# Optimization experiments

Measured on AMD Instinct MI355X. Metric: run time of the kernel, lower is better.

The kernel has to match this reference:

```python
import jax, jax.numpy as jnp
import numpy as np

HDIM = 4
P = 2 ** HDIM  # 16 hypercube nodes


def build_dense_weight(hweight, out_features, in_features):
    # hweight: [hdim+1, P, ob, ib]; assemble dense [out_features, in_features]
    ob = out_features // P
    ib = in_features // P
    i = jnp.arange(P)
    w = jnp.zeros((P, P, ob, ib), dtype=hweight.dtype)
    # diagonal blocks: w[i, i] = hweight[0, i]
    w = w.at[i, i].set(hweight[0])
    # hypercube neighbor blocks: w[i ^ (1<<d), i] = hweight[d+1, i]
    for d in range(HDIM):
        j = i ^ (1 << d)
        w = w.at[j, i].set(hweight[d + 1])
    # permute (0,2,1,3) then reshape -> [out_features, in_features]
    w = jnp.transpose(w, (0, 2, 1, 3)).reshape(out_features, in_features)
    return w


def setup_inputs() -> dict:
    key = jax.random.key(0)
    k1, k2, k3 = jax.random.split(key, 3)
    in_features, out_features = 4096, 4096
    ob = out_features // P
    ib = in_features // P
    x = jax.random.normal(k1, (8192, in_features), dtype=jnp.float32)
    # kaiming-uniform-like scale for the block weights
    bound_w = 1.0 / np.sqrt(ib)
    hweight = jax.random.uniform(k2, (HDIM + 1, P, ob, ib), dtype=jnp.float32,
                                 minval=-bound_w, maxval=bound_w)
    bound_b = 1.0 / np.sqrt(in_features * (HDIM + 1))
    hbias = jax.random.uniform(k3, (out_features,), dtype=jnp.float32,
                               minval=-bound_b, maxval=bound_b)
    return {"x": x, "hweight": hweight, "hbias": hbias}


def reference(x, hweight, hbias):
    out_features = hweight.shape[1] * hweight.shape[2]
    in_features = hweight.shape[1] * hweight.shape[3]
    w = build_dense_weight(hweight, out_features, in_features)
    # F.linear(x, w, b) = x @ w.T + b
    return x @ w.T + hbias
```

## Files before the change

kernel.cpp:

```cpp
#include <hip/hip_runtime.h>

typedef __attribute__((ext_vector_type(8))) short short8;
typedef __attribute__((ext_vector_type(4))) float f32x4;

#define INF 4096
#define NKT 40
#define BUFB 16384

#define AS1 __attribute__((address_space(1)))
#define AS3 __attribute__((address_space(3)))

__device__ __forceinline__ unsigned short f2bf(float f) {
    unsigned int u = __float_as_uint(f);
    u += 0x7FFFu + ((u >> 16) & 1u);
    return (unsigned short)(u >> 16);
}

__device__ __forceinline__ void gl_lds16(const unsigned short* g, void* l) {
    __builtin_amdgcn_global_load_lds((const AS1 void*)g, (AS3 void*)l, 16, 0, 0);
}

__device__ __forceinline__ int swz6(int b) { return b ^ ((b >> 3) & 0x30); }

#define BAR()   __builtin_amdgcn_s_barrier()
#define SB0()   __builtin_amdgcn_sched_barrier(0)

__global__ __launch_bounds__(256)
void cvt_bf16(const float* __restrict__ x, const float* __restrict__ hw,
              unsigned short* __restrict__ xb, unsigned short* __restrict__ wb)
{
    const long long NX = 8192LL * 4096;
    const long long NW = 5LL * 16 * 256 * 256;
    const long long total8 = (NX + NW) / 8;
    for (long long i = (long long)blockIdx.x * 256 + threadIdx.x; i < total8;
         i += (long long)gridDim.x * 256) {
        long long e = i * 8;
        const float* src;
        unsigned short* dst;
        long long off;
        if (e < NX) { src = x;  dst = xb; off = e; }
        else        { src = hw; dst = wb; off = e - NX; }
        float4 f0 = *(const float4*)(src + off);
        float4 f1 = *(const float4*)(src + off + 4);
        ushort4 u0, u1;
        u0.x = f2bf(f0.x); u0.y = f2bf(f0.y); u0.z = f2bf(f0.z); u0.w = f2bf(f0.w);
        u1.x = f2bf(f1.x); u1.y = f2bf(f1.y); u1.z = f2bf(f1.z); u1.w = f2bf(f1.w);
        *(ushort4*)(dst + off)     = u0;
        *(ushort4*)(dst + off + 4) = u1;
    }
}

__global__ __launch_bounds__(256, 3)
void hcl_g128(const unsigned short* __restrict__ xb,
              const unsigned short* __restrict__ wb,
              const float* __restrict__ hb,
              float* __restrict__ out)
{
    __shared__ char lds[3 * BUFB];

    const int tid  = threadIdx.x;
    const int lane = tid & 63;
    const int wave = tid >> 6;
    const int wr   = wave >> 1;
    const int wc   = wave & 1;
    const int ln15 = lane & 15;
    const int hi   = lane >> 4;

    const int newid = (blockIdx.x & 7) * 256 + (blockIdx.x >> 3);
    const int col_i = newid >> 6;
    const int bm0   = (newid & 63) * 128;
    const int p     = col_i >> 1;
    const int nh    = col_i & 1;

    int offA[4], offB[4];
    #pragma unroll
    for (int mf = 0; mf < 4; ++mf)
        offA[mf] = swz6((wr * 64 + mf * 16 + ln15) * 64 + hi * 16);
    #pragma unroll
    for (int nf = 0; nf < 4; ++nf)
        offB[nf] = 8192 + swz6((wc * 64 + nf * 16 + ln15) * 64 + hi * 16);

    int rj[2], cj[2];
    #pragma unroll
    for (int j = 0; j < 2; ++j) {
        int L = swz6(j * 4096 + tid * 16);
        rj[j] = L >> 6;
        cj[j] = (L & 63) >> 1;
    }

    f32x4 acc[4][4] = {};

    auto STAGE = [&](int kt, int buf) {
        if (kt >= NKT) return;
        const int t  = kt >> 3;
        const int s  = p ^ ((1 << t) >> 1);
        const int k0 = (kt & 7) * 32;
        const unsigned short* ga = xb + (size_t)bm0 * INF + s * 256 + k0;
        const unsigned short* gb = wb + ((size_t)(t * 16 + s) << 16) + nh * 128 * 256 + k0;
        char* lb = lds + buf * BUFB + tid * 16;
        gl_lds16(ga + (size_t)rj[0] * INF + cj[0], lb);
        gl_lds16(ga + (size_t)rj[1] * INF + cj[1], lb + 4096);
        gl_lds16(gb + (size_t)rj[0] * 256 + cj[0], lb + 8192);
        gl_lds16(gb + (size_t)rj[1] * 256 + cj[1], lb + 8192 + 4096);
    };

    auto COMPUTE = [&](int buf) {
        const char* L = lds + buf * BUFB;
        short8 fa[4], fb[4];
        #pragma unroll
        for (int nf = 0; nf < 4; ++nf) fb[nf] = *(const short8*)(L + offB[nf]);
        #pragma unroll
        for (int mf = 0; mf < 4; ++mf) fa[mf] = *(const short8*)(L + offA[mf]);
        __builtin_amdgcn_s_setprio(1);
        #pragma unroll
        for (int mi = 0; mi < 4; ++mi)
            #pragma unroll
            for (int nj = 0; nj < 4; ++nj)
                acc[mi][nj] = __builtin_amdgcn_mfma_f32_16x16x32_bf16(
                    fa[mi], fb[nj], acc[mi][nj], 0, 0, 0);
        __builtin_amdgcn_s_setprio(0);
    };

    STAGE(0, 0);
    STAGE(1, 1);
    for (int kt = 0; kt < NKT - 2; ++kt) {
        STAGE(kt + 2, (kt + 2) % 3);
        asm volatile("s_waitcnt vmcnt(8)" ::: "memory");
        BAR(); SB0();
        COMPUTE(kt % 3);
        BAR(); SB0();
    }
    asm volatile("s_waitcnt vmcnt(4)" ::: "memory");
    BAR(); SB0();
    COMPUTE((NKT - 2) % 3);
    BAR(); SB0();
    asm volatile("s_waitcnt vmcnt(0)" ::: "memory");
    BAR(); SB0();
    COMPUTE((NKT - 1) % 3);

    const int col0 = p * 256 + nh * 128 + wc * 64;
    #pragma unroll
    for (int nj = 0; nj < 4; ++nj) {
        const int col = col0 + nj * 16 + ln15;
        const float bias = hb[col];
        #pragma unroll
        for (int mi = 0; mi < 4; ++mi) {
            #pragma unroll
            for (int r = 0; r < 4; ++r) {
                const int row = bm0 + wr * 64 + mi * 16 + hi * 4 + r;
                out[(size_t)row * 4096 + col] = acc[mi][nj][r] + bias;
            }
        }
    }
}

__global__ __launch_bounds__(256)
void hcl_mfma_fused(const float* __restrict__ x,
                    const float* __restrict__ hw,
                    const float* __restrict__ hb,
                    float* __restrict__ out)
{
    __shared__ unsigned short As[128][32];
    __shared__ unsigned short Bs[128][32];

    const int tid  = threadIdx.x;
    const int lane = tid & 63;
    const int wave = tid >> 6;
    const int wr   = wave >> 1, wc = wave & 1;

    const int bm0 = blockIdx.x * 128;
    const int p   = blockIdx.y >> 1;
    const int nh  = blockIdx.y & 1;

    f32x4 acc[4][4] = {};

    const int srow = tid >> 3;
    const int scol = (tid & 7) * 4;

    #pragma unroll
    for (int t = 0; t < 5; ++t) {
        const int mask = (t == 0) ? 0 : (1 << (t - 1));
        const int s = p ^ mask;
        const float* xchunk = x  + (size_t)bm0 * INF + s * 256;
        const float* wchunk = hw + ((size_t)(t * 16 + s) * 256 + nh * 128) * 256;

        for (int k8 = 0; k8 < 8; ++k8) {
            const int kc = k8 * 32;
            #pragma unroll
            for (int i = 0; i < 4; ++i) {
                const int row = i * 32 + srow;
                float4 fa = *(const float4*)(xchunk + (size_t)row * INF + kc + scol);
                float4 fb = *(const float4*)(wchunk + (size_t)row * 256 + kc + scol);
                ushort4 ua, ub;
                ua.x = f2bf(fa.x); ua.y = f2bf(fa.y);
                ua.z = f2bf(fa.z); ua.w = f2bf(fa.w);
                ub.x = f2bf(fb.x); ub.y = f2bf(fb.y);
                ub.z = f2bf(fb.z); ub.w = f2bf(fb.w);
                *(ushort4*)&As[row][scol] = ua;
                *(ushort4*)&Bs[row][scol] = ub;
            }
            __syncthreads();

            short8 a[4], b[4];
            #pragma unroll
            for (int mi = 0; mi < 4; ++mi)
                a[mi] = *(const short8*)&As[wr * 64 + mi * 16 + (lane & 15)][(lane >> 4) * 8];
            #pragma unroll
            for (int nj = 0; nj < 4; ++nj)
                b[nj] = *(const short8*)&Bs[wc * 64 + nj * 16 + (lane & 15)][(lane >> 4) * 8];

            #pragma unroll
            for (int mi = 0; mi < 4; ++mi)
                #pragma unroll
                for (int nj = 0; nj < 4; ++nj)
                    acc[mi][nj] = __builtin_amdgcn_mfma_f32_16x16x32_bf16(
                        a[mi], b[nj], acc[mi][nj], 0, 0, 0);

            __syncthreads();
        }
    }

    const int col0 = p * 256 + nh * 128 + wc * 64;
    #pragma unroll
    for (int nj = 0; nj < 4; ++nj) {
        const int col = col0 + nj * 16 + (lane & 15);
        const float bias = hb[col];
        #pragma unroll
        for (int mi = 0; mi < 4; ++mi) {
            #pragma unroll
            for (int r = 0; r < 4; ++r) {
                const int row = bm0 + wr * 64 + mi * 16 + (lane >> 4) * 4 + r;
                out[(size_t)row * 4096 + col] = acc[mi][nj][r] + bias;
            }
        }
    }
}

extern "C" void kernel_launch(void* const* d_in, const int* in_sizes, int n_in,
                              void* d_out, int out_size, void* d_ws, size_t ws_size,
                              hipStream_t stream) {
    const float* x  = (const float*)d_in[0];
    const float* hw = (const float*)d_in[1];
    const float* hb = (const float*)d_in[2];
    float* out = (float*)d_out;

    const size_t NX = 8192ull * 4096;
    const size_t NW = 5ull * 16 * 256 * 256;
    const size_t need = (NX + NW) * sizeof(unsigned short);

    if (ws_size >= need) {
        unsigned short* xb = (unsigned short*)d_ws;
        unsigned short* wb = xb + NX;
        cvt_bf16<<<2048, 256, 0, stream>>>(x, hw, xb, wb);
        hcl_g128<<<2048, 256, 0, stream>>>(xb, wb, hb, out);
    } else {
        dim3 grid(8192 / 128, 32);
        hcl_mfma_fused<<<grid, 256, 0, stream>>>(x, hw, hb, out);
    }
}
```

Measured before the change: 178.4 us.

## Fuse x fp32-to-bf16 conversion into GEMM A-tile staging, drop separate x cast pass

```diff
diff --git a/kernel.cpp b/kernel.cpp
--- a/kernel.cpp
+++ b/kernel.cpp
@@ -4,8 +4,6 @@
 typedef __attribute__((ext_vector_type(4))) float f32x4;
 
 #define INF 4096
-#define NKT 40
-#define BUFB 16384
 
 #define AS1 __attribute__((address_space(1)))
 #define AS3 __attribute__((address_space(3)))
@@ -16,47 +14,45 @@
     return (unsigned short)(u >> 16);
 }
 
+__device__ __forceinline__ unsigned int pkbf(float a, float b) {
+    unsigned int r;
+    asm volatile("v_cvt_pk_bf16_f32 %0, %1, %2" : "=v"(r) : "v"(a), "v"(b));
+    return r;
+}
+
 __device__ __forceinline__ void gl_lds16(const unsigned short* g, void* l) {
     __builtin_amdgcn_global_load_lds((const AS1 void*)g, (AS3 void*)l, 16, 0, 0);
 }
 
-__device__ __forceinline__ int swz6(int b) { return b ^ ((b >> 3) & 0x30); }
+__device__ __forceinline__ int swz7(int b) { return b ^ ((b >> 3) & 0x70); }
 
 #define BAR()   __builtin_amdgcn_s_barrier()
 #define SB0()   __builtin_amdgcn_sched_barrier(0)
 
 __global__ __launch_bounds__(256)
-void cvt_bf16(const float* __restrict__ x, const float* __restrict__ hw,
-              unsigned short* __restrict__ xb, unsigned short* __restrict__ wb)
+void cvt_w(const float* __restrict__ hw, unsigned short* __restrict__ wb)
 {
-    const long long NX = 8192LL * 4096;
-    const long long NW = 5LL * 16 * 256 * 256;
-    const long long total8 = (NX + NW) / 8;
-    for (long long i = (long long)blockIdx.x * 256 + threadIdx.x; i < total8;
+    const long long NW8 = (5LL * 16 * 256 * 256) / 8;
+    for (long long i = (long long)blockIdx.x * 256 + threadIdx.x; i < NW8;
          i += (long long)gridDim.x * 256) {
         long long e = i * 8;
-        const float* src;
-        unsigned short* dst;
-        long long off;
-        if (e < NX) { src = x;  dst = xb; off = e; }
-        else        { src = hw; dst = wb; off = e - NX; }
-        float4 f0 = *(const float4*)(src + off);
-        float4 f1 = *(const float4*)(src + off + 4);
+        float4 f0 = *(const float4*)(hw + e);
+        float4 f1 = *(const float4*)(hw + e + 4);
         ushort4 u0, u1;
         u0.x = f2bf(f0.x); u0.y = f2bf(f0.y); u0.z = f2bf(f0.z); u0.w = f2bf(f0.w);
         u1.x = f2bf(f1.x); u1.y = f2bf(f1.y); u1.z = f2bf(f1.z); u1.w = f2bf(f1.w);
-        *(ushort4*)(dst + off)     = u0;
-        *(ushort4*)(dst + off + 4) = u1;
-    }
-}
-
-__global__ __launch_bounds__(256, 3)
-void hcl_g128(const unsigned short* __restrict__ xb,
-              const unsigned short* __restrict__ wb,
-              const float* __restrict__ hb,
-              float* __restrict__ out)
+        *(ushort4*)(wb + e)     = u0;
+        *(ushort4*)(wb + e + 4) = u1;
+    }
+}
+
+__global__ __launch_bounds__(256, 2)
+void hcl_f1(const float* __restrict__ x,
+            const unsigned short* __restrict__ wb,
+            const float* __restrict__ hb,
+            float* __restrict__ out)
 {
-    __shared__ char lds[3 * BUFB];
+    __shared__ char lds[2 * 32768];
 
     const int tid  = threadIdx.x;
     const int lane = tid & 63;
@@ -66,77 +62,104 @@
     const int ln15 = lane & 15;
     const int hi   = lane >> 4;
 
-    const int newid = (blockIdx.x & 7) * 256 + (blockIdx.x >> 3);
-    const int col_i = newid >> 6;
-    const int bm0   = (newid & 63) * 128;
-    const int p     = col_i >> 1;
-    const int nh    = col_i & 1;
+    const int bm0 = blockIdx.x * 128;
+    const int p   = blockIdx.y >> 1;
+    const int nh  = blockIdx.y & 1;
 
     int offA[4], offB[4];
     #pragma unroll
     for (int mf = 0; mf < 4; ++mf)
-        offA[mf] = swz6((wr * 64 + mf * 16 + ln15) * 64 + hi * 16);
+        offA[mf] = swz7((wr * 64 + mf * 16 + ln15) * 128 + hi * 16);
     #pragma unroll
     for (int nf = 0; nf < 4; ++nf)
-        offB[nf] = 8192 + swz6((wc * 64 + nf * 16 + ln15) * 64 + hi * 16);
-
-    int rj[2], cj[2];
-    #pragma unroll
-    for (int j = 0; j < 2; ++j) {
-        int L = swz6(j * 4096 + tid * 16);
-        rj[j] = L >> 6;
-        cj[j] = (L & 63) >> 1;
-    }
+        offB[nf] = 16384 + swz7((wc * 64 + nf * 16 + ln15) * 128 + hi * 16);
+
+    const int srow0 = tid >> 3;
+    int scol[4];
+    #pragma unroll
+    for (int j = 0; j < 4; ++j)
+        scol[j] = (swz7(j * 4096 + tid * 16) & 127) >> 1;
 
     f32x4 acc[4][4] = {};
 
-    auto STAGE = [&](int kt, int buf) {
-        if (kt >= NKT) return;
-        const int t  = kt >> 3;
+    auto BSTAGE = [&](int kt) {
+        if (kt >= 20) return;
+        const int t  = kt >> 2;
         const int s  = p ^ ((1 << t) >> 1);
-        const int k0 = (kt & 7) * 32;
-        const unsigned short* ga = xb + (size_t)bm0 * INF + s * 256 + k0;
-        const unsigned short* gb = wb + ((size_t)(t * 16 + s) << 16) + nh * 128 * 256 + k0;
-        char* lb = lds + buf * BUFB + tid * 16;
-        gl_lds16(ga + (size_t)rj[0] * INF + cj[0], lb);
-        gl_lds16(ga + (size_t)rj[1] * INF + cj[1], lb + 4096);
-        gl_lds16(gb + (size_t)rj[0] * 256 + cj[0], lb + 8192);
-        gl_lds16(gb + (size_t)rj[1] * 256 + cj[1], lb + 8192 + 4096);
-    };
-
-    auto COMPUTE = [&](int buf) {
-        const char* L = lds + buf * BUFB;
-        short8 fa[4], fb[4];
-        #pragma unroll
-        for (int nf = 0; nf < 4; ++nf) fb[nf] = *(const short8*)(L + offB[nf]);
-        #pragma unroll
-        for (int mf = 0; mf < 4; ++mf) fa[mf] = *(const short8*)(L + offA[mf]);
+        const int k0 = (kt & 3) * 64;
+        const unsigned short* gb = wb + ((size_t)(t * 16 + s) << 16)
+                                      + (size_t)(nh * 128) * 256 + k0;
+        char* db = lds + (kt & 1) * 32768 + 16384 + tid * 16;
+        #pragma unroll
+        for (int j = 0; j < 4; ++j)
+            gl_lds16(gb + (size_t)(j * 32 + srow0) * 256 + scol[j], db + j * 4096);
+    };
+
+    float4 av[8];
+    auto ALOAD = [&](int kt) {
+        if (kt >= 20) return;
+        const int t  = kt >> 2;
+        const int s  = p ^ ((1 << t) >> 1);
+        const int k0 = (kt & 3) * 64;
+        const float* gx = x + (size_t)bm0 * INF + s * 256 + k0;
+        #pragma unroll
+        for (int j = 0; j < 4; ++j) {
+            const float* src = gx + (size_t)(j * 32 + srow0) * INF + scol[j];
+            av[j * 2 + 0] = *(const float4*)(src);
+            av[j * 2 + 1] = *(const float4*)(src + 4);
+        }
+    };
+    auto AWRITE = [&](int kt) {
+        if (kt >= 20) return;
+        char* da = lds + (kt & 1) * 32768 + tid * 16;
+        #pragma unroll
+        for (int j = 0; j < 4; ++j) {
+            int4 u;
+            u.x = (int)pkbf(av[j * 2 + 0].x, av[j * 2 + 0].y);
+            u.y = (int)pkbf(av[j * 2 + 0].z, av[j * 2 + 0].w);
+            u.z = (int)pkbf(av[j * 2 + 1].x, av[j * 2 + 1].y);
+            u.w = (int)pkbf(av[j * 2 + 1].z, av[j * 2 + 1].w);
+            *(int4*)(da + j * 4096) = u;
+        }
+    };
+
+    auto COMPUTE = [&](int kt) {
+        const char* L = lds + (kt & 1) * 32768;
+        short8 fa[8], fb[8];
+        #pragma unroll
+        for (int nf = 0; nf < 4; ++nf) {
+            fb[nf * 2 + 0] = *(const short8*)(L + offB[nf]);
+            fb[nf * 2 + 1] = *(const short8*)(L + (offB[nf] ^ 64));
+        }
+        #pragma unroll
+        for (int mf = 0; mf < 4; ++mf) {
+            fa[mf * 2 + 0] = *(const short8*)(L + offA[mf]);
+            fa[mf * 2 + 1] = *(const short8*)(L + (offA[mf] ^ 64));
+        }
         __builtin_amdgcn_s_setprio(1);
         #pragma unroll
         for (int mi = 0; mi < 4; ++mi)
             #pragma unroll
             for (int nj = 0; nj < 4; ++nj)
-                acc[mi][nj] = __builtin_amdgcn_mfma_f32_16x16x32_bf16(
-                    fa[mi], fb[nj], acc[mi][nj], 0, 0, 0);
+                #pragma unroll
+                for (int ks = 0; ks < 2; ++ks)
+                    acc[mi][nj] = __builtin_amdgcn_mfma_f32_16x16x32_bf16(
+                        fa[mi * 2 + ks], fb[nj * 2 + ks], acc[mi][nj], 0, 0, 0);
         __builtin_amdgcn_s_setprio(0);
     };
 
-    STAGE(0, 0);
-    STAGE(1, 1);
-    for (int kt = 0; kt < NKT - 2; ++kt) {
-        STAGE(kt + 2, (kt + 2) % 3);
-        asm volatile("s_waitcnt vmcnt(8)" ::: "memory");
+    BSTAGE(0); ALOAD(0);
+    AWRITE(0);
+    asm volatile("s_waitcnt lgkmcnt(0)" ::: "memory");
+
+    for (int kt = 0; kt < 20; ++kt) {
+        BSTAGE(kt + 1); ALOAD(kt + 1);
         BAR(); SB0();
-        COMPUTE(kt % 3);
+        COMPUTE(kt);
+        AWRITE(kt + 1);
+        asm volatile("s_waitcnt lgkmcnt(0)" ::: "memory");
         BAR(); SB0();
     }
-    asm volatile("s_waitcnt vmcnt(4)" ::: "memory");
-    BAR(); SB0();
-    COMPUTE((NKT - 2) % 3);
-    BAR(); SB0();
-    asm volatile("s_waitcnt vmcnt(0)" ::: "memory");
-    BAR(); SB0();
-    COMPUTE((NKT - 1) % 3);
 
     const int col0 = p * 256 + nh * 128 + wc * 64;
     #pragma unroll
@@ -244,15 +267,14 @@
     const float* hb = (const float*)d_in[2];
     float* out = (float*)d_out;
 
-    const size_t NX = 8192ull * 4096;
     const size_t NW = 5ull * 16 * 256 * 256;
-    const size_t need = (NX + NW) * sizeof(unsigned short);
+    const size_t need = NW * sizeof(unsigned short);
 
     if (ws_size >= need) {
-        unsigned short* xb = (unsigned short*)d_ws;
-        unsigned short* wb = xb + NX;
-        cvt_bf16<<<2048, 256, 0, stream>>>(x, hw, xb, wb);
-        hcl_g128<<<2048, 256, 0, stream>>>(xb, wb, hb, out);
+        unsigned short* wbuf = (unsigned short*)d_ws;
+        cvt_w<<<1024, 256, 0, stream>>>(hw, wbuf);
+        dim3 grid(8192 / 128, 32);
+        hcl_f1<<<grid, 256, 0, stream>>>(x, wbuf, hb, out);
     } else {
         dim3 grid(8192 / 128, 32);
         hcl_mfma_fused<<<grid, 256, 0, stream>>>(x, hw, hb, out);
```

Measured after the change: 167.6 us. 6.0% less time.
